# Kernel optimization log

Hardware: AMD Instinct MI355X
Metric: run time of the kernel (lower is better)

Reference implementation:

```python
import jax, jax.numpy as jnp
import numpy as np

N_EMBD = 768
N_EXPERTS = 8
TOP_K = 2
D_FF = 4 * N_EMBD


def setup_inputs() -> dict:
    key = jax.random.key(0)
    k1, k2, k3, k4 = jax.random.split(key, 4)
    x = jax.random.normal(k1, (2, 2048, N_EMBD), dtype=jnp.float32)
    gate_w = jax.random.normal(k2, (N_EMBD, N_EXPERTS), dtype=jnp.float32) * (1.0 / np.sqrt(N_EMBD))
    w_fc = jax.random.normal(k3, (N_EXPERTS, N_EMBD, D_FF), dtype=jnp.float32) * (1.0 / np.sqrt(N_EMBD))
    w_proj = jax.random.normal(k4, (N_EXPERTS, D_FF, N_EMBD), dtype=jnp.float32) * (1.0 / np.sqrt(D_FF))
    return {"x": x, "gate_w": gate_w, "w_fc": w_fc, "w_proj": w_proj}


def reference(x, gate_w, w_fc, w_proj):
    B, S, D = x.shape
    E = w_fc.shape[0]
    xt = x.reshape(-1, D)                    # [T, D]
    T = xt.shape[0]
    scores = xt @ gate_w                      # [T, E]
    expert_weights, expert_indices = jax.lax.top_k(scores, TOP_K)  # [T, K]
    expert_weights = jax.nn.softmax(expert_weights, axis=-1)
    # per-token combine weight for each expert (0 if expert not selected)
    comb = jnp.zeros((T, E), dtype=xt.dtype)
    comb = comb.at[jnp.arange(T)[:, None], expert_indices].add(expert_weights)  # [T, E]
    out = jnp.zeros_like(xt)
    for e in range(E):  # fixed small loop over experts
        h = jax.nn.gelu(xt @ w_fc[e], approximate=False)  # torch nn.GELU default = exact erf
        y_e = h @ w_proj[e]                               # [T, D]
        out = out + comb[:, e:e + 1] * y_e
    return out.reshape(B, S, D)
```

## Files before the change

kernel.cpp:

```cpp
#include <hip/hip_runtime.h>
#include <hip/hip_bf16.h>
#include <math.h>

#define T_TOK 4096
#define D_EMB 768
#define DFF   3072
#define N_EXP 8
#define MAXT  72
#define CNTS  16

typedef __attribute__((ext_vector_type(8))) short bf16x8;
typedef __attribute__((ext_vector_type(4))) float f32x4;

typedef __attribute__((address_space(3))) unsigned int lds_u32_t;
typedef __attribute__((address_space(1))) unsigned int glob_u32_t;

__device__ __forceinline__ void gload16(const void* g, void* l) {
  __builtin_amdgcn_global_load_lds((const glob_u32_t*)g, (lds_u32_t*)l, 16, 0, 0);
}

__device__ __forceinline__ short f2bf(float f) {
  union { __hip_bfloat16 b; short s; } u;
  u.b = __float2bfloat16(f);
  return u.s;
}

__global__ void zero_init_kernel(float4* __restrict__ out4, int n4, int* __restrict__ cnt) {
  int i = blockIdx.x * blockDim.x + threadIdx.x;
  if (i < N_EXP * CNTS) cnt[i] = 0;
  float4 z; z.x = z.y = z.z = z.w = 0.f;
  for (int j = i; j < n4; j += gridDim.x * blockDim.x) out4[j] = z;
}

__global__ void cast_x_kernel(const float4* __restrict__ in, short4* __restrict__ outp, int n4) {
  int i = blockIdx.x * blockDim.x + threadIdx.x;
  if (i >= n4) return;
  float4 v = in[i];
  short4 o;
  o.x = f2bf(v.x); o.y = f2bf(v.y); o.z = f2bf(v.z); o.w = f2bf(v.w);
  outp[i] = o;
}

__global__ void transpose_cast_kernel(const float* __restrict__ in, short* __restrict__ outp,
                                      int R, int C) {
  __shared__ float tile[64][65];
  int e = blockIdx.z;
  int c0 = blockIdx.x * 64, r0 = blockIdx.y * 64;
  const float* src = in + (size_t)e * R * C;
  short* dst = outp + (size_t)e * R * C;
  int tid = threadIdx.x;
#pragma unroll
  for (int it = 0; it < 4; ++it) {
    int idx = tid + it * 256;
    int r = idx >> 4;
    int c4 = idx & 15;
    float4 v = *(const float4*)&src[(size_t)(r0 + r) * C + c0 + c4 * 4];
    tile[r][c4 * 4 + 0] = v.x; tile[r][c4 * 4 + 1] = v.y;
    tile[r][c4 * 4 + 2] = v.z; tile[r][c4 * 4 + 3] = v.w;
  }
  __syncthreads();
#pragma unroll
  for (int it = 0; it < 4; ++it) {
    int idx = tid + it * 256;
    int c = idx >> 4;
    int rr = idx & 15;
    short4 o;
    o.x = f2bf(tile[rr * 4 + 0][c]);
    o.y = f2bf(tile[rr * 4 + 1][c]);
    o.z = f2bf(tile[rr * 4 + 2][c]);
    o.w = f2bf(tile[rr * 4 + 3][c]);
    *(short4*)&dst[(size_t)(c0 + c) * R + r0 + rr * 4] = o;
  }
}

__global__ __launch_bounds__(256)
void gate_kernel(const float* __restrict__ x, const float* __restrict__ gw,
                 int* __restrict__ cnt, int* __restrict__ tok,
                 float* __restrict__ wgt) {
  __shared__ int lcnt[N_EXP];
  __shared__ int gbase[N_EXP];
  __shared__ int le[32];
  __shared__ float lw[32];
  __shared__ int lpos[32];
  int tid = threadIdx.x, lane = tid & 63, wid = tid >> 6;
  if (tid < N_EXP) lcnt[tid] = 0;
  __syncthreads();

#pragma unroll
  for (int i = 0; i < 4; i++) {
    int t = blockIdx.x * 16 + wid * 4 + i;
    float s[N_EXP];
#pragma unroll
    for (int e = 0; e < N_EXP; e++) s[e] = 0.f;
#pragma unroll
    for (int dd = 0; dd < D_EMB / 64; dd++) {
      int d = dd * 64 + lane;
      float xv = x[(size_t)t * D_EMB + d];
#pragma unroll
      for (int e = 0; e < N_EXP; e++) s[e] += xv * gw[d * N_EXP + e];
    }
#pragma unroll
    for (int e = 0; e < N_EXP; e++) {
#pragma unroll
      for (int off = 32; off > 0; off >>= 1) s[e] += __shfl_xor(s[e], off, 64);
    }
    if (lane == 0) {
      int e0 = 0;
#pragma unroll
      for (int e = 1; e < N_EXP; e++) if (s[e] > s[e0]) e0 = e;
      int e1 = -1;
#pragma unroll
      for (int e = 0; e < N_EXP; e++) {
        if (e == e0) continue;
        if (e1 < 0 || s[e] > s[e1]) e1 = e;
      }
      float p1 = __expf(s[e1] - s[e0]);
      float inv = 1.f / (1.f + p1);
      int idx = (wid * 4 + i) * 2;
      le[idx] = e0; lw[idx] = inv;           lpos[idx] = atomicAdd(&lcnt[e0], 1);
      le[idx + 1] = e1; lw[idx + 1] = p1 * inv; lpos[idx + 1] = atomicAdd(&lcnt[e1], 1);
    }
  }
  __syncthreads();
  if (tid < N_EXP) gbase[tid] = atomicAdd(&cnt[tid * CNTS], lcnt[tid]);
  __syncthreads();
  if (tid < 32) {
    int e = le[tid];
    int t = blockIdx.x * 16 + (tid >> 1);
    int p = gbase[e] + lpos[tid];
    tok[e * T_TOK + p] = t;
    wgt[e * T_TOK + p] = lw[tid];
  }
}

__global__ void plan_kernel(const int* __restrict__ cnt, int* __restrict__ offs,
                            int* __restrict__ tile_e, int* __restrict__ tile_rt,
                            int* __restrict__ ntiles) {
  if (threadIdx.x != 0 || blockIdx.x != 0) return;
  int o = 0, nt = 0;
  for (int e = 0; e < N_EXP; e++) {
    offs[e] = o;
    int tc = (cnt[e * CNTS] + 127) >> 7;
    for (int i = 0; i < tc; i++) { tile_e[nt] = e; tile_rt[nt] = i; nt++; }
    o += cnt[e * CNTS];
  }
  *ntiles = nt;
}

template<int KDIM, int NDIM, int SPLITK, int EPI>
__global__ __launch_bounds__(256, 3)
void moe_gemm(const short* __restrict__ A, const short* __restrict__ Bw,
              const int* __restrict__ tok, const float* __restrict__ wgt,
              const int* __restrict__ cnt, const int* __restrict__ offs,
              const int* __restrict__ tile_e, const int* __restrict__ tile_rt,
              const int* __restrict__ ntiles,
              short* __restrict__ hout, float* __restrict__ fout) {
  const int COLT = NDIM / 128;
  const int KS = KDIM / SPLITK;
  const int NKT = KS / 32;
  static_assert(NKT % 3 == 0 && NKT >= 6, "pipeline needs NKT%3==0");

  int nwg = gridDim.x;
  int cpx = nwg >> 3;
  int logical = (blockIdx.x & 7) * cpx + (blockIdx.x >> 3);
  int ct = logical % COLT;
  int tile = (logical / COLT) % MAXT;
  int sk = logical / (COLT * MAXT);
  if (tile >= *ntiles) return;
  int e = tile_e[tile], rt = tile_rt[tile];
  int ne = cnt[e * CNTS];
  int base = offs[e];

  __shared__ __align__(16) short LDS[3 * 2 * 4096];
  short* A0 = LDS;              short* B0 = LDS + 4096;
  short* A1 = LDS + 2 * 4096;   short* B1 = LDS + 3 * 4096;
  short* A2 = LDS + 4 * 4096;   short* B2 = LDS + 5 * 4096;

  int tid = threadIdx.x;
  int lane = tid & 63;
  int wid = tid >> 6;

  const short* aptr0; const short* aptr1;
  const short* bptr0; const short* bptr1;
  int lofs0, lofs1;
  {
    int seg = tid;
    int row = seg >> 2, p = seg & 3;
    int q = p ^ ((row ^ (row >> 2)) & 3);
    int r = rt * 128 + row; if (r >= ne) r = ne - 1;
    size_t ga = (EPI == 0) ? (size_t)tok[e * T_TOK + r] : (size_t)(base + r);
    aptr0 = A + ga * KDIM + sk * KS + q * 8;
    bptr0 = Bw + ((size_t)e * NDIM + ct * 128 + row) * KDIM + sk * KS + q * 8;
    lofs0 = seg * 8;
  }
  {
    int seg = tid + 256;
    int row = seg >> 2, p = seg & 3;
    int q = p ^ ((row ^ (row >> 2)) & 3);
    int r = rt * 128 + row; if (r >= ne) r = ne - 1;
    size_t ga = (EPI == 0) ? (size_t)tok[e * T_TOK + r] : (size_t)(base + r);
    aptr1 = A + ga * KDIM + sk * KS + q * 8;
    bptr1 = Bw + ((size_t)e * NDIM + ct * 128 + row) * KDIM + sk * KS + q * 8;
    lofs1 = seg * 8;
  }

  int wr = (wid >> 1) * 64, wc = (wid & 1) * 64;
  int cb = lane >> 4;

  int offa[4], offb[4];
#pragma unroll
  for (int m = 0; m < 4; m++) {
    int row = wr + m * 16 + (lane & 15);
    offa[m] = row * 32 + (cb ^ ((row ^ (row >> 2)) & 3)) * 8;
  }
#pragma unroll
  for (int n = 0; n < 4; n++) {
    int row = wc + n * 16 + (lane & 15);
    offb[n] = row * 32 + (cb ^ ((row ^ (row >> 2)) & 3)) * 8;
  }

  f32x4 acc[4][4];
#pragma unroll
  for (int m = 0; m < 4; m++)
#pragma unroll
    for (int n = 0; n < 4; n++) acc[m][n] = (f32x4){0.f, 0.f, 0.f, 0.f};

  gload16(aptr0, A0 + lofs0); gload16(bptr0, B0 + lofs0);
  gload16(aptr1, A0 + lofs1); gload16(bptr1, B0 + lofs1);
  gload16(aptr0 + 32, A1 + lofs0); gload16(bptr0 + 32, B1 + lofs0);
  gload16(aptr1 + 32, A1 + lofs1); gload16(bptr1 + 32, B1 + lofs1);

#define VMW(N) do { asm volatile("s_waitcnt vmcnt(" #N ")" ::: "memory"); \
                    __builtin_amdgcn_sched_barrier(0); } while (0)
#define STEP(CA, CB, SA, SB, K0, DOSTAGE, WN) do {                          \
    VMW(WN);                                                                \
    __builtin_amdgcn_s_barrier();                                           \
    if (DOSTAGE) {                                                          \
      gload16(aptr0 + (K0), (SA) + lofs0);                                  \
      gload16(bptr0 + (K0), (SB) + lofs0);                                  \
      gload16(aptr1 + (K0), (SA) + lofs1);                                  \
      gload16(bptr1 + (K0), (SB) + lofs1);                                  \
    }                                                                       \
    bf16x8 af_[4], bv_[4];                                                  \
    _Pragma("unroll") for (int m_ = 0; m_ < 4; ++m_)                        \
      af_[m_] = *(const bf16x8*)((CA) + offa[m_]);                          \
    _Pragma("unroll") for (int n_ = 0; n_ < 4; ++n_)                        \
      bv_[n_] = *(const bf16x8*)((CB) + offb[n_]);                          \
    _Pragma("unroll") for (int m_ = 0; m_ < 4; ++m_)                        \
      _Pragma("unroll") for (int n_ = 0; n_ < 4; ++n_)                      \
        acc[m_][n_] = __builtin_amdgcn_mfma_f32_16x16x32_bf16(              \
            af_[m_], bv_[n_], acc[m_][n_], 0, 0, 0);                        \
  } while (0)

  int kb = 64;
  for (int j = 0; j < NKT / 3 - 1; ++j) {
    STEP(A0, B0, A2, B2, kb,      true, 4);
    STEP(A1, B1, A0, B0, kb + 32, true, 4);
    STEP(A2, B2, A1, B1, kb + 64, true, 4);
    kb += 96;
  }
  STEP(A0, B0, A2, B2, kb, true, 4);
  STEP(A1, B1, A0, B0, 0, false, 4);
  STEP(A2, B2, A1, B1, 0, false, 0);
#undef STEP
#undef VMW

  int colbase = ct * 128 + wc;
#pragma unroll
  for (int m = 0; m < 4; m++) {
#pragma unroll
    for (int j = 0; j < 4; j++) {
      int rloc = rt * 128 + wr + m * 16 + ((lane >> 4) << 2) + j;
      if (rloc < ne) {
        if (EPI == 0) {
          size_t hrow = (size_t)(base + rloc) * NDIM;
#pragma unroll
          for (int n = 0; n < 4; n++) {
            float v = acc[m][n][j];
            float g = 0.5f * v * (1.0f + erff(v * 0.70710678118f));
            hout[hrow + colbase + n * 16 + (lane & 15)] = f2bf(g);
          }
        } else {
          int t = tok[e * T_TOK + rloc];
          float w = wgt[e * T_TOK + rloc];
          float* orow = fout + (size_t)t * NDIM + colbase + (lane & 15);
#pragma unroll
          for (int n = 0; n < 4; n++)
            atomicAdd(orow + n * 16, w * acc[m][n][j]);
        }
      }
    }
  }
}

extern "C" void kernel_launch(void* const* d_in, const int* in_sizes, int n_in,
                              void* d_out, int out_size, void* d_ws, size_t ws_size,
                              hipStream_t stream) {
  const float* x   = (const float*)d_in[0];
  const float* gw  = (const float*)d_in[1];
  const float* wfc = (const float*)d_in[2];
  const float* wpj = (const float*)d_in[3];
  float* out = (float*)d_out;

  char* ws = (char*)d_ws;
  const size_t SZ_XB = (size_t)T_TOK * D_EMB * 2;
  const size_t SZ_W  = (size_t)N_EXP * D_EMB * DFF * 2;
  const size_t SZ_H  = (size_t)2 * T_TOK * DFF * 2;
  short* xb   = (short*)(ws);
  short* wfcT = (short*)(ws + SZ_XB);
  short* wpjT = (short*)(ws + SZ_XB + SZ_W);
  short* h    = (short*)(ws + SZ_XB + 2 * SZ_W);
  char* p2    = ws + SZ_XB + 2 * SZ_W + SZ_H;
  int*   tok  = (int*)(p2);
  float* wgt  = (float*)(p2 + (size_t)N_EXP * T_TOK * 4);
  char* p3    = p2 + (size_t)N_EXP * T_TOK * 8;
  int*   cnt     = (int*)(p3);
  int*   offs    = (int*)(p3 + 1024);
  int*   tile_e  = (int*)(p3 + 1024 + 64);
  int*   tile_rt = (int*)(p3 + 1024 + 64 + 512);
  int*   ntiles  = (int*)(p3 + 1024 + 64 + 1024);

  int n4 = out_size / 4;
  zero_init_kernel<<<2048, 256, 0, stream>>>((float4*)out, n4, cnt);
  cast_x_kernel<<<(T_TOK * D_EMB / 4 + 255) / 256, 256, 0, stream>>>(
      (const float4*)x, (short4*)xb, T_TOK * D_EMB / 4);
  transpose_cast_kernel<<<dim3(DFF / 64, D_EMB / 64, N_EXP), 256, 0, stream>>>(wfc, wfcT, D_EMB, DFF);
  transpose_cast_kernel<<<dim3(D_EMB / 64, DFF / 64, N_EXP), 256, 0, stream>>>(wpj, wpjT, DFF, D_EMB);
  gate_kernel<<<T_TOK / 16, 256, 0, stream>>>(x, gw, cnt, tok, wgt);
  plan_kernel<<<1, 1, 0, stream>>>(cnt, offs, tile_e, tile_rt, ntiles);
  moe_gemm<D_EMB, DFF, 1, 0><<<MAXT * (DFF / 128), 256, 0, stream>>>(
      xb, wfcT, tok, wgt, cnt, offs, tile_e, tile_rt, ntiles, h, nullptr);
  moe_gemm<DFF, D_EMB, 2, 1><<<2 * MAXT * (D_EMB / 128), 256, 0, stream>>>(
      h, wpjT, tok, wgt, cnt, offs, tile_e, tile_rt, ntiles, nullptr, out);
}
```

Measured before the change: 233.6 us.

## Replace direct global-to-LDS loads with register-staged pipeline, swap MFMA operands, tanh GELU

Drops the global_load_lds path and instead stages tiles through registers with two alternating register sets written into a triple-buffered LDS ring, unrolled by six K-steps. The MFMA operand order is swapped so each lane holds four consecutive output columns. This lets the epilogue pack bf16 pairs into 8-byte vector stores instead of scalar 2-byte stores. GELU switches from exact erf to a tanh approximation built on __expf, trading accuracy against the exact-erf reference for cheaper math.

```diff
diff --git a/kernel.cpp b/kernel.cpp
--- a/kernel.cpp
+++ b/kernel.cpp
@@ -12,17 +12,19 @@
 typedef __attribute__((ext_vector_type(8))) short bf16x8;
 typedef __attribute__((ext_vector_type(4))) float f32x4;
 
-typedef __attribute__((address_space(3))) unsigned int lds_u32_t;
-typedef __attribute__((address_space(1))) unsigned int glob_u32_t;
-
-__device__ __forceinline__ void gload16(const void* g, void* l) {
-  __builtin_amdgcn_global_load_lds((const glob_u32_t*)g, (lds_u32_t*)l, 16, 0, 0);
-}
-
 __device__ __forceinline__ short f2bf(float f) {
   union { __hip_bfloat16 b; short s; } u;
   u.b = __float2bfloat16(f);
   return u.s;
+}
+
+__device__ __forceinline__ float gelu_f(float v) {
+  float u = 0.7978845608f * v * (1.0f + 0.044715f * v * v);
+  float a = fabsf(u);
+  float em = __expf(-2.0f * a);
+  float th = (1.0f - em) / (1.0f + em);
+  th = (u < 0.0f) ? -th : th;
+  return 0.5f * v * (1.0f + th);
 }
 
 __global__ void zero_init_kernel(float4* __restrict__ out4, int n4, int* __restrict__ cnt) {
@@ -158,7 +160,7 @@
   const int COLT = NDIM / 128;
   const int KS = KDIM / SPLITK;
   const int NKT = KS / 32;
-  static_assert(NKT % 3 == 0 && NKT >= 6, "pipeline needs NKT%3==0");
+  static_assert(NKT % 6 == 0 && NKT >= 12, "pipeline needs NKT%6==0");
 
   int nwg = gridDim.x;
   int cpx = nwg >> 3;
@@ -171,10 +173,7 @@
   int ne = cnt[e * CNTS];
   int base = offs[e];
 
-  __shared__ __align__(16) short LDS[3 * 2 * 4096];
-  short* A0 = LDS;              short* B0 = LDS + 4096;
-  short* A1 = LDS + 2 * 4096;   short* B1 = LDS + 3 * 4096;
-  short* A2 = LDS + 4 * 4096;   short* B2 = LDS + 5 * 4096;
+  __shared__ __align__(16) short A0[4096], B0[4096], A1[4096], B1[4096], A2[4096], B2[4096];
 
   int tid = threadIdx.x;
   int lane = tid & 63;
@@ -225,69 +224,84 @@
 #pragma unroll
     for (int n = 0; n < 4; n++) acc[m][n] = (f32x4){0.f, 0.f, 0.f, 0.f};
 
-  gload16(aptr0, A0 + lofs0); gload16(bptr0, B0 + lofs0);
-  gload16(aptr1, A0 + lofs1); gload16(bptr1, B0 + lofs1);
-  gload16(aptr0 + 32, A1 + lofs0); gload16(bptr0 + 32, B1 + lofs0);
-  gload16(aptr1 + 32, A1 + lofs1); gload16(bptr1 + 32, B1 + lofs1);
-
-#define VMW(N) do { asm volatile("s_waitcnt vmcnt(" #N ")" ::: "memory"); \
-                    __builtin_amdgcn_sched_barrier(0); } while (0)
-#define STEP(CA, CB, SA, SB, K0, DOSTAGE, WN) do {                          \
-    VMW(WN);                                                                \
-    __builtin_amdgcn_s_barrier();                                           \
-    if (DOSTAGE) {                                                          \
-      gload16(aptr0 + (K0), (SA) + lofs0);                                  \
-      gload16(bptr0 + (K0), (SB) + lofs0);                                  \
-      gload16(aptr1 + (K0), (SA) + lofs1);                                  \
-      gload16(bptr1 + (K0), (SB) + lofs1);                                  \
-    }                                                                       \
-    bf16x8 af_[4], bv_[4];                                                  \
-    _Pragma("unroll") for (int m_ = 0; m_ < 4; ++m_)                        \
-      af_[m_] = *(const bf16x8*)((CA) + offa[m_]);                          \
-    _Pragma("unroll") for (int n_ = 0; n_ < 4; ++n_)                        \
-      bv_[n_] = *(const bf16x8*)((CB) + offb[n_]);                          \
-    _Pragma("unroll") for (int m_ = 0; m_ < 4; ++m_)                        \
-      _Pragma("unroll") for (int n_ = 0; n_ < 4; ++n_)                      \
-        acc[m_][n_] = __builtin_amdgcn_mfma_f32_16x16x32_bf16(              \
-            af_[m_], bv_[n_], acc[m_][n_], 0, 0, 0);                        \
+  f32x4 s0a0, s0a1, s0b0, s0b1;
+  f32x4 s1a0, s1a1, s1b0, s1b1;
+
+#define LOADS0(K0) do { s0a0 = *(const f32x4*)(aptr0 + (K0)); s0a1 = *(const f32x4*)(aptr1 + (K0)); \
+                        s0b0 = *(const f32x4*)(bptr0 + (K0)); s0b1 = *(const f32x4*)(bptr1 + (K0)); } while (0)
+#define LOADS1(K0) do { s1a0 = *(const f32x4*)(aptr0 + (K0)); s1a1 = *(const f32x4*)(aptr1 + (K0)); \
+                        s1b0 = *(const f32x4*)(bptr0 + (K0)); s1b1 = *(const f32x4*)(bptr1 + (K0)); } while (0)
+#define WR0(AW, BW) do { *(f32x4*)((AW) + lofs0) = s0a0; *(f32x4*)((AW) + lofs1) = s0a1; \
+                         *(f32x4*)((BW) + lofs0) = s0b0; *(f32x4*)((BW) + lofs1) = s0b1; } while (0)
+#define WR1(AW, BW) do { *(f32x4*)((AW) + lofs0) = s1a0; *(f32x4*)((AW) + lofs1) = s1a1; \
+                         *(f32x4*)((BW) + lofs0) = s1b0; *(f32x4*)((BW) + lofs1) = s1b1; } while (0)
+#define BAR() do { __builtin_amdgcn_sched_barrier(0); __builtin_amdgcn_s_barrier(); \
+                   __builtin_amdgcn_sched_barrier(0); } while (0)
+#define COMPUTE(AR, BR) do {                                                   \
+    bf16x8 af_[4], bv_[4];                                                     \
+    _Pragma("unroll") for (int m_ = 0; m_ < 4; ++m_)                           \
+      af_[m_] = *(const bf16x8*)((AR) + offa[m_]);                             \
+    _Pragma("unroll") for (int n_ = 0; n_ < 4; ++n_)                           \
+      bv_[n_] = *(const bf16x8*)((BR) + offb[n_]);                             \
+    _Pragma("unroll") for (int m_ = 0; m_ < 4; ++m_)                           \
+      _Pragma("unroll") for (int n_ = 0; n_ < 4; ++n_)                         \
+        acc[m_][n_] = __builtin_amdgcn_mfma_f32_16x16x32_bf16(                 \
+            bv_[n_], af_[m_], acc[m_][n_], 0, 0, 0);                           \
   } while (0)
 
+  LOADS0(0);
+  LOADS1(32);
+  WR0(A0, B0);
+
   int kb = 64;
-  for (int j = 0; j < NKT / 3 - 1; ++j) {
-    STEP(A0, B0, A2, B2, kb,      true, 4);
-    STEP(A1, B1, A0, B0, kb + 32, true, 4);
-    STEP(A2, B2, A1, B1, kb + 64, true, 4);
-    kb += 96;
-  }
-  STEP(A0, B0, A2, B2, kb, true, 4);
-  STEP(A1, B1, A0, B0, 0, false, 4);
-  STEP(A2, B2, A1, B1, 0, false, 0);
-#undef STEP
-#undef VMW
-
-  int colbase = ct * 128 + wc;
+  for (int g = 0; g < (NKT - 6) / 6; ++g) {
+    LOADS0(kb +   0); WR1(A1, B1); BAR(); COMPUTE(A0, B0);
+    LOADS1(kb +  32); WR0(A2, B2); BAR(); COMPUTE(A1, B1);
+    LOADS0(kb +  64); WR1(A0, B0); BAR(); COMPUTE(A2, B2);
+    LOADS1(kb +  96); WR0(A1, B1); BAR(); COMPUTE(A0, B0);
+    LOADS0(kb + 128); WR1(A2, B2); BAR(); COMPUTE(A1, B1);
+    LOADS1(kb + 160); WR0(A0, B0); BAR(); COMPUTE(A2, B2);
+    kb += 192;
+  }
+  LOADS0(kb +   0); WR1(A1, B1); BAR(); COMPUTE(A0, B0);
+  LOADS1(kb +  32); WR0(A2, B2); BAR(); COMPUTE(A1, B1);
+  LOADS0(kb +  64); WR1(A0, B0); BAR(); COMPUTE(A2, B2);
+  LOADS1(kb +  96); WR0(A1, B1); BAR(); COMPUTE(A0, B0);
+  WR1(A2, B2);      BAR(); COMPUTE(A1, B1);
+  BAR(); COMPUTE(A2, B2);
+
+#undef LOADS0
+#undef LOADS1
+#undef WR0
+#undef WR1
+#undef BAR
+#undef COMPUTE
+
+  int colq = ct * 128 + wc + ((lane >> 4) << 2);
 #pragma unroll
   for (int m = 0; m < 4; m++) {
-#pragma unroll
-    for (int j = 0; j < 4; j++) {
-      int rloc = rt * 128 + wr + m * 16 + ((lane >> 4) << 2) + j;
-      if (rloc < ne) {
-        if (EPI == 0) {
-          size_t hrow = (size_t)(base + rloc) * NDIM;
-#pragma unroll
-          for (int n = 0; n < 4; n++) {
-            float v = acc[m][n][j];
-            float g = 0.5f * v * (1.0f + erff(v * 0.70710678118f));
-            hout[hrow + colbase + n * 16 + (lane & 15)] = f2bf(g);
-          }
-        } else {
-          int t = tok[e * T_TOK + rloc];
-          float w = wgt[e * T_TOK + rloc];
-          float* orow = fout + (size_t)t * NDIM + colbase + (lane & 15);
-#pragma unroll
-          for (int n = 0; n < 4; n++)
-            atomicAdd(orow + n * 16, w * acc[m][n][j]);
+    int rloc = rt * 128 + wr + m * 16 + (lane & 15);
+    if (rloc < ne) {
+      if (EPI == 0) {
+        size_t hrow = (size_t)(base + rloc) * NDIM;
+#pragma unroll
+        for (int n = 0; n < 4; n++) {
+          unsigned int lo = (unsigned short)f2bf(gelu_f(acc[m][n][0])) |
+                            ((unsigned int)(unsigned short)f2bf(gelu_f(acc[m][n][1])) << 16);
+          unsigned int hi = (unsigned short)f2bf(gelu_f(acc[m][n][2])) |
+                            ((unsigned int)(unsigned short)f2bf(gelu_f(acc[m][n][3])) << 16);
+          uint2 v; v.x = lo; v.y = hi;
+          *(uint2*)&hout[hrow + colq + n * 16] = v;
         }
+      } else {
+        int t = tok[e * T_TOK + rloc];
+        float w = wgt[e * T_TOK + rloc];
+        float* orow = fout + (size_t)t * NDIM + colq;
+#pragma unroll
+        for (int n = 0; n < 4; n++)
+#pragma unroll
+          for (int j = 0; j < 4; j++)
+            atomicAdd(orow + n * 16 + j, w * acc[m][n][j]);
       }
     }
   }
```

Measured after the change: 350.0 us. +49.8%, slower.
